# Optimization experiments

Measured on AMD Instinct MI355X. Metric: run time of the kernel, lower is better.

The kernel has to match this reference:

```python
import jax, jax.numpy as jnp
import numpy as np

N_NODES = 50000
N_EDGES = 600000
H = 128


def setup_inputs() -> dict:
    key = jax.random.key(0)
    ks = jax.random.split(key, 7)
    node_emb = jax.random.normal(ks[0], (N_NODES, H), dtype=jnp.float32)
    # PyTorch Linear default init ~ U(-1/sqrt(fan_in), 1/sqrt(fan_in)); scaled normal is fine for a baseline
    W1 = jax.random.normal(ks[1], (H, 2 * H), dtype=jnp.float32) * (1.0 / np.sqrt(2 * H))
    b1 = jax.random.normal(ks[2], (H,), dtype=jnp.float32) * 0.01
    W2 = jax.random.normal(ks[3], (1, H), dtype=jnp.float32) * (1.0 / np.sqrt(H))
    b2 = jax.random.normal(ks[4], (1,), dtype=jnp.float32) * 0.01
    src = jax.random.randint(ks[5], (N_EDGES,), 0, N_NODES, dtype=jnp.int64)
    dst = jax.random.randint(ks[6], (N_EDGES,), 0, N_NODES, dtype=jnp.int64)
    return {"node_emb": node_emb, "W1": W1, "b1": b1, "W2": W2, "b2": b2,
            "src": src, "dst": dst}


def reference(node_emb, W1, b1, W2, b2, src, dst):
    # gather per-edge endpoint embeddings and concat -> [E, 2H]
    h = jnp.concatenate([node_emb[src], node_emb[dst]], axis=1)
    # 2-layer MLP: Linear(2H->H) -> ReLU -> Linear(H->1) -> squeeze
    hidden = jax.nn.relu(h @ W1.T + b1)          # [E, H]
    scores = hidden @ W2.T + b2                   # [E, 1]
    return scores[:, 0]                           # [E]
```

## Files before the change

### kernel.cpp

```cpp
#include <hip/hip_runtime.h>
#include <hip/hip_bf16.h>


#define H   128
#define NJJ 256
#define BM  32
#define EPW 32
#define CPAD_F32 260

typedef __attribute__((ext_vector_type(8))) short  frag_ab;
typedef __attribute__((ext_vector_type(4))) float  f32x4;
typedef __attribute__((ext_vector_type(4))) unsigned int   uint4v;

__device__ __forceinline__ unsigned short f2bf(float x) {
    unsigned int u = __float_as_uint(x);
    unsigned int r = u + 0x7FFFu + ((u >> 16) & 1u);
    return (unsigned short)(r >> 16);
}

__device__ __forceinline__ unsigned int pk_bf16(float lo, float hi) {
    unsigned int r;
    asm("v_cvt_pk_bf16_f32 %0, %1, %2" : "=v"(r) : "v"(lo), "v"(hi));
    return r;
}

__device__ __forceinline__ frag_ab relu_sum(uint4v s, uint4v d) {
    uint4v r;
#pragma unroll
    for (int p = 0; p < 4; ++p) {
        float sl = __uint_as_float(s[p] << 16);
        float sh = __uint_as_float(s[p] & 0xFFFF0000u);
        float dl = __uint_as_float(d[p] << 16);
        float dh = __uint_as_float(d[p] & 0xFFFF0000u);
        float l = sl + dl; l = l > 0.f ? l : 0.f;
        float h = sh + dh; h = h > 0.f ? h : 0.f;
        r[p] = pk_bf16(l, h);
    }
    return __builtin_bit_cast(frag_ab, r);
}

__global__ __launch_bounds__(256)
void convert_weights(const float* __restrict__ W1, const float* __restrict__ W2,
                     unsigned short* __restrict__ W1f, unsigned short* __restrict__ W2c) {
    if (blockIdx.x == 128) {
        if (threadIdx.x < H) W2c[threadIdx.x] = f2bf(W2[threadIdx.x]);
        return;
    }
    int idx = blockIdx.x * 256 + threadIdx.x;
    int e     = idx & 7;
    int chunk = idx >> 3;
    int lane  = chunk & 63;
    int ks    = (chunk >> 6) & 3;
    int cf    = (chunk >> 8) & 3;
    int wid   = chunk >> 10;
    int col   = wid * 64 + (lane & 15) + cf * 16;
    int k     = ks * 32 + (lane >> 4) * 8 + e;
    W1f[idx] = f2bf(W1[(size_t)(col & 127) * 256 + (size_t)(col >> 7) * H + k]);
}

__global__ __launch_bounds__(256)
void precompute_P_mfma(const float* __restrict__ emb,
                       const unsigned short* __restrict__ W1f,
                       const float* __restrict__ b1,
                       unsigned short* __restrict__ P,
                       int n_nodes) {
    __shared__ __align__(16) float ldsC[BM * CPAD_F32];
    int tid  = threadIdx.x;
    int lane = tid & 63;
    int wid  = tid >> 6;
    int block0 = blockIdx.x * BM;
    if (block0 + BM > n_nodes) block0 = n_nodes - BM;
    if (block0 < 0) block0 = 0;

    const frag_ab* wf = (const frag_ab*)W1f;
    frag_ab Bf[4][4];
#pragma unroll
    for (int cf = 0; cf < 4; ++cf)
#pragma unroll
        for (int ks = 0; ks < 4; ++ks)
            Bf[cf][ks] = wf[(((size_t)wid * 4 + cf) * 4 + ks) * 64 + lane];

    f32x4 acc[2][4];
#pragma unroll
    for (int mf = 0; mf < 2; ++mf)
#pragma unroll
        for (int cf = 0; cf < 4; ++cf) acc[mf][cf] = (f32x4){0.f, 0.f, 0.f, 0.f};

    int row16 = lane & 15;
    int g     = lane >> 4;
    const float* a0 = emb + (size_t)(block0 + row16) * H + g * 8;

#pragma unroll
    for (int ks = 0; ks < 4; ++ks) {
        frag_ab Af[2];
#pragma unroll
        for (int mf = 0; mf < 2; ++mf) {
            const float4* p = (const float4*)(a0 + mf * 16 * H + ks * 32);
            float4 a = p[0], b = p[1];
            uint4v w;
            w[0] = pk_bf16(a.x, a.y);
            w[1] = pk_bf16(a.z, a.w);
            w[2] = pk_bf16(b.x, b.y);
            w[3] = pk_bf16(b.z, b.w);
            Af[mf] = __builtin_bit_cast(frag_ab, w);
        }
#pragma unroll
        for (int mf = 0; mf < 2; ++mf)
#pragma unroll
            for (int cf = 0; cf < 4; ++cf)
                acc[mf][cf] = __builtin_amdgcn_mfma_f32_16x16x32_bf16(
                    Af[mf], Bf[cf][ks], acc[mf][cf], 0, 0, 0);
    }

    {
        int colbase = wid * 64 + row16;
        int rbase   = g * 4;
        float b1c[4];
#pragma unroll
        for (int cf = 0; cf < 4; ++cf) {
            int col = colbase + cf * 16;
            b1c[cf] = (col < H) ? b1[col] : 0.f;
        }
#pragma unroll
        for (int mf = 0; mf < 2; ++mf)
#pragma unroll
            for (int cf = 0; cf < 4; ++cf) {
                int col = colbase + cf * 16;
#pragma unroll
                for (int r = 0; r < 4; ++r) {
                    int row = mf * 16 + rbase + r;
                    ldsC[row * CPAD_F32 + col] = acc[mf][cf][r] + b1c[cf];
                }
            }
    }
    __syncthreads();

#pragma unroll
    for (int it = 0; it < 4; ++it) {
        int c   = it * 256 + tid;
        int row = c >> 5;
        int off = c & 31;
        const float4* s = (const float4*)(ldsC + row * CPAD_F32 + off * 8);
        float4 x = s[0], y = s[1];
        uint4v o;
        o[0] = pk_bf16(x.x, x.y);
        o[1] = pk_bf16(x.z, x.w);
        o[2] = pk_bf16(y.x, y.y);
        o[3] = pk_bf16(y.z, y.w);
        *(uint4v*)((char*)P + (size_t)(block0 + row) * 512 + off * 16) = o;
    }
}

__global__ __launch_bounds__(256)
void edge_score_mfma(const unsigned short* __restrict__ P,
                     const unsigned short* __restrict__ W2c,
                     const float* __restrict__ b2,
                     const int* __restrict__ src,
                     const int* __restrict__ dst,
                     float* __restrict__ out,
                     int n_edges) {
    int lane = threadIdx.x & 63;
    int wave = blockIdx.x * 4 + (threadIdx.x >> 6);
    int e0 = wave * EPW;
    if (e0 >= n_edges) return;

    frag_ab Bf[4];
    {
        int krun = (lane >> 4) * 8;
#pragma unroll
        for (int ks = 0; ks < 4; ++ks)
            Bf[ks] = *(const frag_ab*)(W2c + ks * 32 + krun);
    }
    float b2v = b2[0];
    int el = lane & 15;
    int kb = (lane >> 4) * 16;

    int eA = e0 + el;       if (eA > n_edges - 1) eA = n_edges - 1;
    int eB = e0 + 16 + el;  if (eB > n_edges - 1) eB = n_edges - 1;
    const char* pb = (const char*)P;
    const char* sA = pb + (size_t)src[eA] * 512 + kb;
    const char* dA = pb + (size_t)dst[eA] * 512 + 256 + kb;
    const char* sB = pb + (size_t)src[eB] * 512 + kb;
    const char* dB = pb + (size_t)dst[eB] * 512 + 256 + kb;

    uint4v rsA[4], rdA[4], rsB[4], rdB[4];
#pragma unroll
    for (int ks = 0; ks < 4; ++ks) {
        rsA[ks] = *(const uint4v*)(sA + ks * 64);
        rdA[ks] = *(const uint4v*)(dA + ks * 64);
        rsB[ks] = *(const uint4v*)(sB + ks * 64);
        rdB[ks] = *(const uint4v*)(dB + ks * 64);
    }

    f32x4 accA = (f32x4){0.f, 0.f, 0.f, 0.f};
    f32x4 accB = (f32x4){0.f, 0.f, 0.f, 0.f};
#pragma unroll
    for (int ks = 0; ks < 4; ++ks) {
        accA = __builtin_amdgcn_mfma_f32_16x16x32_bf16(relu_sum(rsA[ks], rdA[ks]), Bf[ks], accA, 0, 0, 0);
        accB = __builtin_amdgcn_mfma_f32_16x16x32_bf16(relu_sum(rsB[ks], rdB[ks]), Bf[ks], accB, 0, 0, 0);
    }

    if (el == 0) {
        int r0 = (lane >> 4) * 4;
        int ea = e0 + r0, eb = e0 + 16 + r0;
        float4 oA = { accA[0] + b2v, accA[1] + b2v, accA[2] + b2v, accA[3] + b2v };
        float4 oB = { accB[0] + b2v, accB[1] + b2v, accB[2] + b2v, accB[3] + b2v };
        if (eb + 3 < n_edges) {
            *(float4*)(out + ea) = oA;
            *(float4*)(out + eb) = oB;
        } else {
#pragma unroll
            for (int r = 0; r < 4; ++r) {
                if (ea + r < n_edges) out[ea + r] = accA[r] + b2v;
                if (eb + r < n_edges) out[eb + r] = accB[r] + b2v;
            }
        }
    }
}

__global__ __launch_bounds__(128)
void naive_edge(const float* __restrict__ emb,
                const float* __restrict__ W1,
                const float* __restrict__ b1,
                const float* __restrict__ W2,
                const float* __restrict__ b2,
                const int* __restrict__ src,
                const int* __restrict__ dst,
                float* __restrict__ out,
                int n_edges) {
    __shared__ float es[H], ed[H];
    __shared__ float red[2];
    int e = blockIdx.x;
    if (e >= n_edges) return;
    int j = threadIdx.x;
    int s = src[e], d = dst[e];
    es[j] = emb[(size_t)s * H + j];
    ed[j] = emb[(size_t)d * H + j];
    __syncthreads();
    const float* w = W1 + (size_t)j * 256;
    float acc = b1[j];
    for (int k = 0; k < H; ++k) acc += es[k] * w[k] + ed[k] * w[H + k];
    acc = acc > 0.f ? acc : 0.f;
    float p = acc * W2[j];
#pragma unroll
    for (int off = 32; off; off >>= 1) p += __shfl_xor(p, off, 64);
    int lane = j & 63, wid = j >> 6;
    if (lane == 0) red[wid] = p;
    __syncthreads();
    if (j == 0) out[e] = red[0] + red[1] + b2[0];
}

extern "C" void kernel_launch(void* const* d_in, const int* in_sizes, int n_in,
                              void* d_out, int out_size, void* d_ws, size_t ws_size,
                              hipStream_t stream) {
    const float* emb = (const float*)d_in[0];
    const float* W1  = (const float*)d_in[1];
    const float* b1  = (const float*)d_in[2];
    const float* W2  = (const float*)d_in[3];
    const float* b2  = (const float*)d_in[4];
    const int*   src = (const int*)d_in[5];
    const int*   dst = (const int*)d_in[6];
    float* out = (float*)d_out;

    int n_nodes = in_sizes[0] / H;
    int n_edges = in_sizes[5];

    size_t needP = (size_t)n_nodes * NJJ * sizeof(unsigned short);
    size_t offW1 = (needP + 255) & ~(size_t)255;
    size_t offW2 = offW1 + (size_t)NJJ * H * sizeof(unsigned short);
    size_t need  = offW2 + 256;

    if (ws_size >= need && n_nodes >= BM) {
        unsigned short* P   = (unsigned short*)d_ws;
        unsigned short* W1f = (unsigned short*)((char*)d_ws + offW1);
        unsigned short* W2c = (unsigned short*)((char*)d_ws + offW2);
        convert_weights<<<129, 256, 0, stream>>>(W1, W2, W1f, W2c);
        int grid1 = (n_nodes + BM - 1) / BM;
        precompute_P_mfma<<<grid1, 256, 0, stream>>>(emb, W1f, b1, P, n_nodes);
        int grid2 = (n_edges + EPW * 4 - 1) / (EPW * 4);
        edge_score_mfma<<<grid2, 256, 0, stream>>>(P, W2c, b2, src, dst, out, n_edges);
    } else {
        naive_edge<<<n_edges, 128, 0, stream>>>(emb, W1, b1, W2, b2, src, dst, out, n_edges);
    }
}
```

Baseline: 73.02 us.

## Stage node embedding tile into LDS via async global_load_lds with XOR swizzle

Each block now copies its 32x128 fp32 embedding tile into shared memory with direct global-to-LDS loads using fully coalesced 16-byte chunks, swizzled by XOR of chunk and row to avoid bank conflicts. The MFMA A-fragments are then read from LDS instead of strided global float4 loads, and the LDS buffer is reused for the output staging. The aim is better coalescing of the embedding reads in the per-node precompute kernel, at the cost of an extra barrier and the time taken to fill LDS.

```diff
diff --git a/kernel.cpp b/kernel.cpp
--- a/kernel.cpp
+++ b/kernel.cpp
@@ -58,13 +58,20 @@
     W1f[idx] = f2bf(W1[(size_t)(col & 127) * 256 + (size_t)(col >> 7) * H + k]);
 }
 
+__device__ __forceinline__ int swz_chunk(int c, int row) {
+    return (c & ~7) | ((c ^ row) & 7);
+}
+
 __global__ __launch_bounds__(256)
 void precompute_P_mfma(const float* __restrict__ emb,
                        const unsigned short* __restrict__ W1f,
                        const float* __restrict__ b1,
                        unsigned short* __restrict__ P,
                        int n_nodes) {
-    __shared__ __align__(16) float ldsC[BM * CPAD_F32];
+    __shared__ __align__(1024) float ldsbuf[BM * CPAD_F32];
+    float* ldsA = ldsbuf;
+    float* ldsC = ldsbuf;
+
     int tid  = threadIdx.x;
     int lane = tid & 63;
     int wid  = tid >> 6;
@@ -80,6 +87,21 @@
         for (int ks = 0; ks < 4; ++ks)
             Bf[cf][ks] = wf[(((size_t)wid * 4 + cf) * 4 + ks) * 64 + lane];
 
+    {
+#pragma unroll
+        for (int j = 0; j < 4; ++j) {
+            int row = wid * 8 + j * 2 + (lane >> 5);
+            int cp  = lane & 31;
+            int c   = swz_chunk(cp, row);
+            const float* g = emb + (size_t)(block0 + row) * H + c * 4;
+            void* l = (char*)ldsA + wid * 4096 + j * 1024;
+            __builtin_amdgcn_global_load_lds(
+                (const __attribute__((address_space(1))) void*)g,
+                (__attribute__((address_space(3))) void*)l, 16, 0, 0);
+        }
+    }
+    __syncthreads();
+
     f32x4 acc[2][4];
 #pragma unroll
     for (int mf = 0; mf < 2; ++mf)
@@ -87,21 +109,22 @@
         for (int cf = 0; cf < 4; ++cf) acc[mf][cf] = (f32x4){0.f, 0.f, 0.f, 0.f};
 
     int row16 = lane & 15;
-    int g     = lane >> 4;
-    const float* a0 = emb + (size_t)(block0 + row16) * H + g * 8;
-
+    int g4    = lane >> 4;
 #pragma unroll
     for (int ks = 0; ks < 4; ++ks) {
         frag_ab Af[2];
 #pragma unroll
         for (int mf = 0; mf < 2; ++mf) {
-            const float4* p = (const float4*)(a0 + mf * 16 * H + ks * 32);
-            float4 a = p[0], b = p[1];
+            int row   = mf * 16 + row16;
+            int cbase = ks * 8 + g4 * 2;
+            const char* base = (const char*)ldsA + row * 512;
+            float4 x = *(const float4*)(base + (swz_chunk(cbase,     row) << 4));
+            float4 y = *(const float4*)(base + (swz_chunk(cbase + 1, row) << 4));
             uint4v w;
-            w[0] = pk_bf16(a.x, a.y);
-            w[1] = pk_bf16(a.z, a.w);
-            w[2] = pk_bf16(b.x, b.y);
-            w[3] = pk_bf16(b.z, b.w);
+            w[0] = pk_bf16(x.x, x.y);
+            w[1] = pk_bf16(x.z, x.w);
+            w[2] = pk_bf16(y.x, y.y);
+            w[3] = pk_bf16(y.z, y.w);
             Af[mf] = __builtin_bit_cast(frag_ab, w);
         }
 #pragma unroll
@@ -112,9 +135,11 @@
                     Af[mf], Bf[cf][ks], acc[mf][cf], 0, 0, 0);
     }
 
+    __syncthreads();
+
     {
         int colbase = wid * 64 + row16;
-        int rbase   = g * 4;
+        int rbase   = g4 * 4;
         float b1c[4];
 #pragma unroll
         for (int cf = 0; cf < 4; ++cf) {
```

Result: faster. 64.41 us (-11.8%).
